# Kernel optimization log

Hardware: AMD Instinct MI355X
Metric: run time of the kernel (lower is better)

The kernel has to match this reference:

```python
import jax, jax.numpy as jnp
import numpy as np

EPS = 1e-20

def squash(s):
    # n = ||s||; out = (1 - 1/(exp(n)+eps)) * s/(n+eps)
    n = jnp.linalg.norm(s, axis=-1, keepdims=True)
    return (1.0 - 1.0 / (jnp.exp(n) + EPS)) * (s / (n + EPS))

def setup_inputs() -> dict:
    key = jax.random.key(0)
    k1, k2 = jax.random.split(key)
    B, K, J, I, Z = 128, 32, 1152, 8, 16
    x = jax.random.normal(k1, (B, J, I), dtype=jnp.float32)
    # kaiming_normal_ fan_in init for W
    W = jax.random.normal(k2, (K, J, I, Z), dtype=jnp.float32) * np.float32(np.sqrt(2.0 / (J * I)))
    b = jnp.zeros((K, J, 1), dtype=jnp.float32)
    return {"x": x, "W": W, "b": b}

def reference(x, W, b):
    Z = W.shape[-1]
    # capsule transform: u[b,k,j,z] = sum_i x[b,j,i] * W[k,j,i,z]
    u = jnp.einsum('bji,kjiz->bkjz', x, W)
    # self-similarity: c[b,k,i] = sum_{j,z} u[b,k,i,z]*u[b,k,j,z]
    #                            = sum_z u[b,k,i,z] * (sum_j u[b,k,j,z])
    c = jnp.einsum('bkjz,bkz->bkj', u, u.sum(axis=2))[..., None]
    c = c / jnp.sqrt(jnp.asarray(Z, dtype=u.dtype))
    c = jax.nn.softmax(c, axis=1) + b  # softmax over caps2 (K) axis
    s = jnp.sum(u * c, axis=-2)  # [B, K, Z]
    return squash(s)
```

## Files before the change

kernel.cpp:

```cpp
#include <hip/hip_runtime.h>
#include <hip/hip_bf16.h>
#include <math.h>

#define BB 128
#define KK 32
#define JJ 1152
#define II 8
#define ZZ 16

#define NJSA 48
#define NJT  144

typedef __attribute__((ext_vector_type(8))) short short8;
typedef __attribute__((ext_vector_type(4))) float floatx4;

#define N_USUM  (KK * BB * ZZ)
#define N_USUMP (NJSA * KK * BB * ZZ)
#define N_SACCP ((size_t)NJT * KK * BB * ZZ)

#define KX_BLOCKS ((JJ * BB) / 256)
#define KW_BLOCKS ((KK * JJ * ZZ) / 256)

__device__ __forceinline__ float bf2f(short h) {
    unsigned int w = ((unsigned int)(unsigned short)h) << 16;
    float f; __builtin_memcpy(&f, &w, 4);
    return f;
}

extern "C" __global__ __launch_bounds__(256)
void kP(const float* __restrict__ x, const float* __restrict__ W,
        __hip_bfloat16* __restrict__ xbf, __hip_bfloat16* __restrict__ Wt) {
    if (blockIdx.x < KX_BLOCKS) {
        int idx = blockIdx.x * 256 + threadIdx.x;
        int j_in = idx & 15;
        int rest = idx >> 4;
        int b    = rest & 127;
        int j    = (rest >> 7) * 16 + j_in;
        const float4* xp = (const float4*)(x + ((size_t)b * JJ + j) * II);
        float4 a = xp[0], c = xp[1];
        union { short8 v; __hip_bfloat16 h[8]; } u;
        u.h[0] = __float2bfloat16(a.x); u.h[1] = __float2bfloat16(a.y);
        u.h[2] = __float2bfloat16(a.z); u.h[3] = __float2bfloat16(a.w);
        u.h[4] = __float2bfloat16(c.x); u.h[5] = __float2bfloat16(c.y);
        u.h[6] = __float2bfloat16(c.z); u.h[7] = __float2bfloat16(c.w);
        *(short8*)(xbf + ((size_t)j * BB + b) * II) = u.v;
    } else {
        int idx = (blockIdx.x - KX_BLOCKS) * 256 + threadIdx.x;
        int z    = idx & 15;
        int rest = idx >> 4;
        int j    = rest % JJ;
        int k    = rest / JJ;
        const float* src = W + (((size_t)k * JJ + j) * II) * ZZ + z;
        union { short8 v; __hip_bfloat16 h[8]; } u;
#pragma unroll
        for (int i = 0; i < II; ++i) u.h[i] = __float2bfloat16(src[i * ZZ]);
        *(short8*)(Wt + (((size_t)k * JJ + j) * ZZ + z) * II) = u.v;
    }
}

extern "C" __global__ __launch_bounds__(64)
void kA(const __hip_bfloat16* __restrict__ xbf,
        const __hip_bfloat16* __restrict__ Wt, float* __restrict__ usum_p) {
    const int kt = blockIdx.x;
    const int bt = blockIdx.y;
    const int js = blockIdx.z;
    const int l  = threadIdx.x;
    const int n  = l & 15;
    const int g  = l >> 4;
    const int b1 = bt * 32 + n;
    const int b2 = b1 + 16;

    short8 xv1[6], xv2[6];
#pragma unroll
    for (int q = 0; q < 6; ++q) {
        int j = (js * 6 + q) * 4 + g;
        xv1[q] = *(const short8*)(xbf + ((size_t)j * BB + b1) * II);
        xv2[q] = *(const short8*)(xbf + ((size_t)j * BB + b2) * II);
    }

    floatx4 acc1[4], acc2[4];
#pragma unroll
    for (int kk = 0; kk < 4; ++kk) {
        acc1[kk] = (floatx4){0.f, 0.f, 0.f, 0.f};
        acc2[kk] = (floatx4){0.f, 0.f, 0.f, 0.f};
    }

#pragma unroll
    for (int kk = 0; kk < 4; ++kk) {
        const int k = kt * 4 + kk;
#pragma unroll
        for (int q = 0; q < 6; ++q) {
            int j = (js * 6 + q) * 4 + g;
            short8 a = *(const short8*)(Wt + (((size_t)k * JJ + j) * ZZ + n) * II);
            acc1[kk] = __builtin_amdgcn_mfma_f32_16x16x32_bf16(a, xv1[q], acc1[kk], 0, 0, 0);
            acc2[kk] = __builtin_amdgcn_mfma_f32_16x16x32_bf16(a, xv2[q], acc2[kk], 0, 0, 0);
        }
    }
#pragma unroll
    for (int kk = 0; kk < 4; ++kk) {
        const int k = kt * 4 + kk;
        *(floatx4*)(usum_p + (((size_t)js * KK + k) * BB + b1) * ZZ + g * 4) = acc1[kk];
        *(floatx4*)(usum_p + (((size_t)js * KK + k) * BB + b2) * ZZ + g * 4) = acc2[kk];
    }
}

extern "C" __global__ __launch_bounds__(256)
void kR(const float* __restrict__ usum_p, float* __restrict__ usum) {
    int p   = blockIdx.x * 256 + threadIdx.x;
    int r   = p & 3;
    int idx = p >> 2;
    floatx4 s = (floatx4){0.f, 0.f, 0.f, 0.f};
#pragma unroll 4
    for (int js = r * 12; js < r * 12 + 12; ++js)
        s += *(const floatx4*)(usum_p + (size_t)js * N_USUM + (size_t)idx * 4);
#pragma unroll
    for (int c = 0; c < 4; ++c) {
        s[c] += __shfl_xor(s[c], 1);
        s[c] += __shfl_xor(s[c], 2);
    }
    if (r == 0) *(floatx4*)(usum + (size_t)idx * 4) = s;
}

extern "C" __global__ __launch_bounds__(256)
void kBC(const __hip_bfloat16* __restrict__ xbf,
         const __hip_bfloat16* __restrict__ Wt,
         const float* __restrict__ usum, const float* __restrict__ bias,
         float* __restrict__ sacc_p) {
    __shared__ float eS[KK * 8 * 32];
    __shared__ float Sw[4 * 8 * 32];
    __shared__ float rS[8 * 32];

    const int jt = blockIdx.x;
    const int bt = blockIdx.y;
    const int t  = threadIdx.x;
    const int w  = t >> 6;
    const int l  = t & 63;
    const int n  = l & 15;
    const int g  = l >> 4;
    const int b1 = bt * 32 + n;
    const int b2 = b1 + 16;
    const int j0 = jt * 8;

    short8 xv1[8], xv2[8];
#pragma unroll
    for (int jl = 0; jl < 8; ++jl) {
        xv1[jl] = *(const short8*)(xbf + ((size_t)(j0 + jl) * BB + b1) * II);
        xv2[jl] = *(const short8*)(xbf + ((size_t)(j0 + jl) * BB + b2) * II);
    }

    float Sacc1[8], Sacc2[8];
#pragma unroll
    for (int jl = 0; jl < 8; ++jl) { Sacc1[jl] = 0.f; Sacc2[jl] = 0.f; }

#pragma unroll 2
    for (int kk = 0; kk < 8; ++kk) {
        const int k = w * 8 + kk;
        floatx4 us1 = *(const floatx4*)(usum + ((size_t)k * BB + b1) * ZZ + g * 4);
        floatx4 us2 = *(const floatx4*)(usum + ((size_t)k * BB + b2) * ZZ + g * 4);
#pragma unroll
        for (int jl = 0; jl < 8; ++jl) {
            short8 a = *(const short8*)(Wt + (((size_t)k * JJ + j0 + jl) * ZZ + n) * II);
            floatx4 c0 = {0.f, 0.f, 0.f, 0.f};
            floatx4 u1 = __builtin_amdgcn_mfma_f32_16x16x32_bf16(a, xv1[jl], c0, 0, 0, 0);
            floatx4 u2 = __builtin_amdgcn_mfma_f32_16x16x32_bf16(a, xv2[jl], c0, 0, 0, 0);
            float dp1 = u1[0] * us1[0];
            dp1 = fmaf(u1[1], us1[1], dp1);
            dp1 = fmaf(u1[2], us1[2], dp1);
            dp1 = fmaf(u1[3], us1[3], dp1);
            float dp2 = u2[0] * us2[0];
            dp2 = fmaf(u2[1], us2[1], dp2);
            dp2 = fmaf(u2[2], us2[2], dp2);
            dp2 = fmaf(u2[3], us2[3], dp2);
            dp1 += __shfl_xor(dp1, 16);
            dp1 += __shfl_xor(dp1, 32);
            dp2 += __shfl_xor(dp2, 16);
            dp2 += __shfl_xor(dp2, 32);
            float e1 = __expf(dp1 * 0.0625f);
            float e2 = __expf(dp2 * 0.0625f);
            Sacc1[jl] += e1;
            Sacc2[jl] += e2;
            if (g == 0) {
                eS[(k * 8 + jl) * 32 + n]      = e1;
                eS[(k * 8 + jl) * 32 + n + 16] = e2;
            }
        }
    }
    if (g == 0) {
#pragma unroll
        for (int jl = 0; jl < 8; ++jl) {
            Sw[(w * 8 + jl) * 32 + n]      = Sacc1[jl];
            Sw[(w * 8 + jl) * 32 + n + 16] = Sacc2[jl];
        }
    }
    __syncthreads();
    {
        int jl = t >> 5, col = t & 31;
        float s = Sw[(0 * 8 + jl) * 32 + col] + Sw[(1 * 8 + jl) * 32 + col]
                + Sw[(2 * 8 + jl) * 32 + col] + Sw[(3 * 8 + jl) * 32 + col];
        rS[jl * 32 + col] = __builtin_amdgcn_rcpf(s);
    }
    __syncthreads();

    float xf1[2][8], xf2[2][8];
#pragma unroll
    for (int quad = 0; quad < 2; ++quad) {
        union { short8 v; short s[8]; } xr1, xr2;
        int j = j0 + quad * 4 + g;
        xr1.v = *(const short8*)(xbf + ((size_t)j * BB + b1) * II);
        xr2.v = *(const short8*)(xbf + ((size_t)j * BB + b2) * II);
#pragma unroll
        for (int i = 0; i < II; ++i) {
            xf1[quad][i] = bf2f(xr1.s[i]);
            xf2[quad][i] = bf2f(xr2.s[i]);
        }
    }

    floatx4 acc1[8], acc2[8];
#pragma unroll
    for (int kk = 0; kk < 8; ++kk) {
        acc1[kk] = (floatx4){0.f, 0.f, 0.f, 0.f};
        acc2[kk] = (floatx4){0.f, 0.f, 0.f, 0.f};
    }

#pragma unroll 2
    for (int kk = 0; kk < 8; ++kk) {
        const int k = w * 8 + kk;
#pragma unroll
        for (int quad = 0; quad < 2; ++quad) {
            const int jl = quad * 4 + g;
            const int j  = j0 + jl;
            float bj = bias[(size_t)k * JJ + j];
            float c1 = fmaf(eS[(k * 8 + jl) * 32 + n],      rS[jl * 32 + n],      bj);
            float c2 = fmaf(eS[(k * 8 + jl) * 32 + n + 16], rS[jl * 32 + n + 16], bj);
            union { short8 v; short s[8]; } xs1, xs2;
#pragma unroll
            for (int i = 0; i < II; ++i) {
                __hip_bfloat16 h1 = __float2bfloat16(xf1[quad][i] * c1);
                __hip_bfloat16 h2 = __float2bfloat16(xf2[quad][i] * c2);
                __builtin_memcpy(&xs1.s[i], &h1, 2);
                __builtin_memcpy(&xs2.s[i], &h2, 2);
            }
            short8 a = *(const short8*)(Wt + (((size_t)k * JJ + j) * ZZ + n) * II);
            acc1[kk] = __builtin_amdgcn_mfma_f32_16x16x32_bf16(a, xs1.v, acc1[kk], 0, 0, 0);
            acc2[kk] = __builtin_amdgcn_mfma_f32_16x16x32_bf16(a, xs2.v, acc2[kk], 0, 0, 0);
        }
    }
#pragma unroll
    for (int kk = 0; kk < 8; ++kk) {
        const int k = w * 8 + kk;
        *(floatx4*)(sacc_p + (((size_t)jt * KK + k) * BB + b1) * ZZ + g * 4) = acc1[kk];
        *(floatx4*)(sacc_p + (((size_t)jt * KK + k) * BB + b2) * ZZ + g * 4) = acc2[kk];
    }
}

extern "C" __global__ __launch_bounds__(256)
void kD(const float* __restrict__ sacc_p, float* __restrict__ out) {
    int p  = blockIdx.x * 256 + threadIdx.x;
    int r  = p & 3;
    int q  = (p >> 2) & 3;
    int kb = p >> 4;
    int k  = kb >> 7;
    int b  = kb & 127;

    floatx4 v = (floatx4){0.f, 0.f, 0.f, 0.f};
#pragma unroll 6
    for (int jt = r * 36; jt < r * 36 + 36; ++jt)
        v += *(const floatx4*)(sacc_p + (((size_t)jt * KK + k) * BB + b) * ZZ + q * 4);

#pragma unroll
    for (int c = 0; c < 4; ++c) {
        v[c] += __shfl_xor(v[c], 1);
        v[c] += __shfl_xor(v[c], 2);
    }

    float nsq = v[0] * v[0];
    nsq = fmaf(v[1], v[1], nsq);
    nsq = fmaf(v[2], v[2], nsq);
    nsq = fmaf(v[3], v[3], nsq);
    nsq += __shfl_xor(nsq, 4);
    nsq += __shfl_xor(nsq, 8);

    float nr = sqrtf(nsq);
    float scale = (1.f - 1.f / (__expf(nr) + 1e-20f)) / (nr + 1e-20f);
    if (r == 0) {
        floatx4 o = v * scale;
        *(floatx4*)(out + ((size_t)b * KK + k) * ZZ + q * 4) = o;
    }
}

extern "C" void kernel_launch(void* const* d_in, const int* in_sizes, int n_in,
                              void* d_out, int out_size, void* d_ws, size_t ws_size,
                              hipStream_t stream) {
    const float* x    = (const float*)d_in[0];
    const float* W    = (const float*)d_in[1];
    const float* bias = (const float*)d_in[2];
    float*       out  = (float*)d_out;

    float* ws     = (float*)d_ws;
    float* usum   = ws;
    float* usum_p = usum + N_USUM;
    float* sacc_p = usum_p + N_USUMP;
    __hip_bfloat16* xbf = (__hip_bfloat16*)(sacc_p + N_SACCP);
    __hip_bfloat16* Wt  = xbf + (size_t)JJ * BB * II;


    kP<<<KX_BLOCKS + KW_BLOCKS, 256, 0, stream>>>(x, W, xbf, Wt);
    kA<<<dim3(8, 4, NJSA), 64, 0, stream>>>(xbf, Wt, usum_p);
    kR<<<(KK * BB * ZZ) / 256, 256, 0, stream>>>(usum_p, usum);
    kBC<<<dim3(NJT, 4), 256, 0, stream>>>(xbf, Wt, usum, bias, sacc_p);
    kD<<<(KK * BB * 16) / 256, 256, 0, stream>>>(sacc_p, out);
}
```

Measured before the change: 132.4 us.

## Reduce kA partials in shared memory and split kBC over eight waves

kA now runs four waves per block, each covering a different slice of j. Their partial u-sums are combined in shared memory before being written out, which cuts the usum_p partial buffer from 48 to 12 slices and lightens the kR reduction. kBC doubles its block to 512 threads, so each wave handles 4 capsules instead of 8. This adds parallelism and reduces per-thread accumulator registers, at the cost of a larger cross-wave sum of softmax denominators and more shared-memory traffic.

```diff
diff --git a/kernel.cpp b/kernel.cpp
--- a/kernel.cpp
+++ b/kernel.cpp
@@ -8,14 +8,14 @@
 #define II 8
 #define ZZ 16
 
-#define NJSA 48
+#define NJG  12
 #define NJT  144
 
 typedef __attribute__((ext_vector_type(8))) short short8;
 typedef __attribute__((ext_vector_type(4))) float floatx4;
 
 #define N_USUM  (KK * BB * ZZ)
-#define N_USUMP (NJSA * KK * BB * ZZ)
+#define N_USUMP (NJG * KK * BB * ZZ)
 #define N_SACCP ((size_t)NJT * KK * BB * ZZ)
 
 #define KX_BLOCKS ((JJ * BB) / 256)
@@ -58,22 +58,26 @@
     }
 }
 
-extern "C" __global__ __launch_bounds__(64)
+extern "C" __global__ __launch_bounds__(256)
 void kA(const __hip_bfloat16* __restrict__ xbf,
         const __hip_bfloat16* __restrict__ Wt, float* __restrict__ usum_p) {
+    __shared__ float Ls[4][8][256];
     const int kt = blockIdx.x;
     const int bt = blockIdx.y;
-    const int js = blockIdx.z;
-    const int l  = threadIdx.x;
+    const int jg = blockIdx.z;
+    const int t  = threadIdx.x;
+    const int w  = t >> 6;
+    const int l  = t & 63;
     const int n  = l & 15;
     const int g  = l >> 4;
     const int b1 = bt * 32 + n;
     const int b2 = b1 + 16;
+    const int q0 = jg * 24 + w * 6;
 
     short8 xv1[6], xv2[6];
 #pragma unroll
     for (int q = 0; q < 6; ++q) {
-        int j = (js * 6 + q) * 4 + g;
+        int j = (q0 + q) * 4 + g;
         xv1[q] = *(const short8*)(xbf + ((size_t)j * BB + b1) * II);
         xv2[q] = *(const short8*)(xbf + ((size_t)j * BB + b2) * II);
     }
@@ -90,7 +94,7 @@
         const int k = kt * 4 + kk;
 #pragma unroll
         for (int q = 0; q < 6; ++q) {
-            int j = (js * 6 + q) * 4 + g;
+            int j = (q0 + q) * 4 + g;
             short8 a = *(const short8*)(Wt + (((size_t)k * JJ + j) * ZZ + n) * II);
             acc1[kk] = __builtin_amdgcn_mfma_f32_16x16x32_bf16(a, xv1[q], acc1[kk], 0, 0, 0);
             acc2[kk] = __builtin_amdgcn_mfma_f32_16x16x32_bf16(a, xv2[q], acc2[kk], 0, 0, 0);
@@ -98,9 +102,23 @@
     }
 #pragma unroll
     for (int kk = 0; kk < 4; ++kk) {
-        const int k = kt * 4 + kk;
-        *(floatx4*)(usum_p + (((size_t)js * KK + k) * BB + b1) * ZZ + g * 4) = acc1[kk];
-        *(floatx4*)(usum_p + (((size_t)js * KK + k) * BB + b2) * ZZ + g * 4) = acc2[kk];
+        *(floatx4*)&Ls[w][kk * 2 + 0][l * 4] = acc1[kk];
+        *(floatx4*)&Ls[w][kk * 2 + 1][l * 4] = acc2[kk];
+    }
+    __syncthreads();
+#pragma unroll
+    for (int pp = 0; pp < 2; ++pp) {
+        int p  = t + pp * 256;
+        int s  = p >> 6;
+        int ll = p & 63;
+        int nn = ll & 15, gg = ll >> 4;
+        floatx4 v = *(const floatx4*)&Ls[0][s][ll * 4];
+        v += *(const floatx4*)&Ls[1][s][ll * 4];
+        v += *(const floatx4*)&Ls[2][s][ll * 4];
+        v += *(const floatx4*)&Ls[3][s][ll * 4];
+        int k = kt * 4 + (s >> 1);
+        int b = bt * 32 + nn + 16 * (s & 1);
+        *(floatx4*)(usum_p + (((size_t)jg * KK + k) * BB + b) * ZZ + gg * 4) = v;
     }
 }
 
@@ -110,9 +128,9 @@
     int r   = p & 3;
     int idx = p >> 2;
     floatx4 s = (floatx4){0.f, 0.f, 0.f, 0.f};
-#pragma unroll 4
-    for (int js = r * 12; js < r * 12 + 12; ++js)
-        s += *(const floatx4*)(usum_p + (size_t)js * N_USUM + (size_t)idx * 4);
+#pragma unroll
+    for (int jg = r * 3; jg < r * 3 + 3; ++jg)
+        s += *(const floatx4*)(usum_p + (size_t)jg * N_USUM + (size_t)idx * 4);
 #pragma unroll
     for (int c = 0; c < 4; ++c) {
         s[c] += __shfl_xor(s[c], 1);
@@ -121,13 +139,13 @@
     if (r == 0) *(floatx4*)(usum + (size_t)idx * 4) = s;
 }
 
-extern "C" __global__ __launch_bounds__(256)
+extern "C" __global__ __launch_bounds__(512)
 void kBC(const __hip_bfloat16* __restrict__ xbf,
          const __hip_bfloat16* __restrict__ Wt,
          const float* __restrict__ usum, const float* __restrict__ bias,
          float* __restrict__ sacc_p) {
     __shared__ float eS[KK * 8 * 32];
-    __shared__ float Sw[4 * 8 * 32];
+    __shared__ float Sw[8 * 8 * 32];
     __shared__ float rS[8 * 32];
 
     const int jt = blockIdx.x;
@@ -153,8 +171,8 @@
     for (int jl = 0; jl < 8; ++jl) { Sacc1[jl] = 0.f; Sacc2[jl] = 0.f; }
 
 #pragma unroll 2
-    for (int kk = 0; kk < 8; ++kk) {
-        const int k = w * 8 + kk;
+    for (int kk = 0; kk < 4; ++kk) {
+        const int k = w * 4 + kk;
         floatx4 us1 = *(const floatx4*)(usum + ((size_t)k * BB + b1) * ZZ + g * 4);
         floatx4 us2 = *(const floatx4*)(usum + ((size_t)k * BB + b2) * ZZ + g * 4);
 #pragma unroll
@@ -193,10 +211,11 @@
         }
     }
     __syncthreads();
-    {
+    if (t < 256) {
         int jl = t >> 5, col = t & 31;
-        float s = Sw[(0 * 8 + jl) * 32 + col] + Sw[(1 * 8 + jl) * 32 + col]
-                + Sw[(2 * 8 + jl) * 32 + col] + Sw[(3 * 8 + jl) * 32 + col];
+        float s = 0.f;
+#pragma unroll
+        for (int ww = 0; ww < 8; ++ww) s += Sw[(ww * 8 + jl) * 32 + col];
         rS[jl * 32 + col] = __builtin_amdgcn_rcpf(s);
     }
     __syncthreads();
@@ -215,16 +234,16 @@
         }
     }
 
-    floatx4 acc1[8], acc2[8];
-#pragma unroll
-    for (int kk = 0; kk < 8; ++kk) {
+    floatx4 acc1[4], acc2[4];
+#pragma unroll
+    for (int kk = 0; kk < 4; ++kk) {
         acc1[kk] = (floatx4){0.f, 0.f, 0.f, 0.f};
         acc2[kk] = (floatx4){0.f, 0.f, 0.f, 0.f};
     }
 
 #pragma unroll 2
-    for (int kk = 0; kk < 8; ++kk) {
-        const int k = w * 8 + kk;
+    for (int kk = 0; kk < 4; ++kk) {
+        const int k = w * 4 + kk;
 #pragma unroll
         for (int quad = 0; quad < 2; ++quad) {
             const int jl = quad * 4 + g;
@@ -246,8 +265,8 @@
         }
     }
 #pragma unroll
-    for (int kk = 0; kk < 8; ++kk) {
-        const int k = w * 8 + kk;
+    for (int kk = 0; kk < 4; ++kk) {
+        const int k = w * 4 + kk;
         *(floatx4*)(sacc_p + (((size_t)jt * KK + k) * BB + b1) * ZZ + g * 4) = acc1[kk];
         *(floatx4*)(sacc_p + (((size_t)jt * KK + k) * BB + b2) * ZZ + g * 4) = acc2[kk];
     }
@@ -305,8 +324,8 @@
 
 
     kP<<<KX_BLOCKS + KW_BLOCKS, 256, 0, stream>>>(x, W, xbf, Wt);
-    kA<<<dim3(8, 4, NJSA), 64, 0, stream>>>(xbf, Wt, usum_p);
+    kA<<<dim3(8, 4, NJG), 256, 0, stream>>>(xbf, Wt, usum_p);
     kR<<<(KK * BB * ZZ) / 256, 256, 0, stream>>>(usum_p, usum);
-    kBC<<<dim3(NJT, 4), 256, 0, stream>>>(xbf, Wt, usum, bias, sacc_p);
+    kBC<<<dim3(NJT, 4), 512, 0, stream>>>(xbf, Wt, usum, bias, sacc_p);
     kD<<<(KK * BB * 16) / 256, 256, 0, stream>>>(sacc_p, out);
 }
```

New measurement: 146.5 us. 10.6% more time.
